# Kernel tuning notes

Hardware: AMD Instinct MI355X
Metric: run time of the kernel (lower is better)

## Reference

```python
import jax, jax.numpy as jnp
import numpy as np

CHANNELS = 256
TEMPERATURE = 0.1
VAR_LAMBDA = 0.001
N = 4096


def _pairwise_sq_dist(x, y):
    xx = jnp.sum(x * x, axis=-1)[:, None]
    yy = jnp.sum(y * y, axis=-1)[None, :]
    xy = jnp.einsum('ic,jc->ij', x, y)
    return xx + yy - 2.0 * xy


def _tcc_loss(emb_a, emb_b, idxes):
    scale = 1.0 / (CHANNELS * TEMPERATURE)
    sim_ab = -_pairwise_sq_dist(emb_a, emb_b) * scale            # [Na, Nb]
    softmaxed_sim_ab = jax.nn.softmax(sim_ab, axis=-1)
    soft_nn = softmaxed_sim_ab @ emb_b                            # [Na, C]
    sim_ba = -_pairwise_sq_dist(soft_nn, emb_a) * scale           # [Na, Na]
    beta = jax.nn.softmax(sim_ba, axis=-1)
    preds = jnp.sum(beta * idxes, axis=-1, keepdims=True)         # [Na, 1]
    pred_var = jnp.sum((idxes - preds) ** 2 * beta, axis=1)       # [Na]
    pred_var_log = jnp.log(pred_var)
    squared_error = (idxes - jnp.squeeze(preds, -1)) ** 2
    return jnp.sum(jnp.exp(-pred_var_log) * squared_error + VAR_LAMBDA * pred_var_log)


def setup_inputs() -> dict:
    key = jax.random.key(0)
    k1, k2 = jax.random.split(key)
    emb_a = jax.random.normal(k1, (1, N, CHANNELS), dtype=jnp.float32)
    emb_b = jax.random.normal(k2, (1, N, CHANNELS), dtype=jnp.float32)
    idx_a = jnp.arange(N, dtype=jnp.float32)
    idx_b = jnp.arange(N, dtype=jnp.float32)
    return {"emb_a": emb_a, "emb_b": emb_b, "idx_a": idx_a, "idx_b": idx_b}


def reference(emb_a, emb_b, idx_a, idx_b):
    a = jnp.squeeze(emb_a, 0)
    b = jnp.squeeze(emb_b, 0)
    loss_ab = _tcc_loss(a, b, idx_a)
    loss_ba = _tcc_loss(b, a, idx_b)
    return (loss_ab + loss_ba) / (a.shape[0] + b.shape[0])
```

## Files before the change

kernel.cpp:

```cpp
#include <hip/hip_runtime.h>

#define NTOT 4096
#define CH 256
#define SCALE 0.0390625f
#define LAM 0.001f

typedef unsigned short u16;
typedef __attribute__((ext_vector_type(8))) short short8;
typedef __attribute__((ext_vector_type(4))) float floatx4;

__device__ __forceinline__ float wave_sum64(float v) {
  #pragma unroll
  for (int o = 32; o; o >>= 1) v += __shfl_down(v, o, 64);
  return v;
}
__device__ __forceinline__ u16 f2bf(float f) {
  unsigned u = __float_as_uint(f);
  u += 0x7fffu + ((u >> 16) & 1u);
  return (u16)(u >> 16);
}
__device__ __forceinline__ float bf2f(u16 h) {
  return __uint_as_float(((unsigned)h) << 16);
}
__device__ __forceinline__ void gload_lds(const u16* g, void* l) {
  __builtin_amdgcn_global_load_lds((const __attribute__((address_space(1))) void*)g,
                                   (__attribute__((address_space(3))) void*)l, 16, 0, 0);
}
__device__ __forceinline__ void mm4x4(const short8 (&av)[4], const short8 (&bv)[4],
                                      floatx4 (&acc)[4][4]) {
  #pragma unroll
  for (int m = 0; m < 4; ++m)
    #pragma unroll
    for (int n = 0; n < 4; ++n)
      acc[m][n] = __builtin_amdgcn_mfma_f32_16x16x32_bf16(av[m], bv[n], acc[m][n], 0, 0, 0);
}

__global__ __launch_bounds__(64) void cvt_norm_k(const float* __restrict__ a,
                                                 const float* __restrict__ b,
                                                 u16* __restrict__ ab, u16* __restrict__ bb,
                                                 float* __restrict__ na, float* __restrict__ nb) {
  int row = blockIdx.x;
  const float* src; u16* dst; float* nd;
  if (row < NTOT) { src = a; dst = ab; nd = na; }
  else { row -= NTOT; src = b; dst = bb; nd = nb; }
  const float4 v = *reinterpret_cast<const float4*>(src + (size_t)row * CH + threadIdx.x * 4);
  const u16 h0 = f2bf(v.x), h1 = f2bf(v.y), h2 = f2bf(v.z), h3 = f2bf(v.w);
  uint2 st;
  st.x = (unsigned)h0 | ((unsigned)h1 << 16);
  st.y = (unsigned)h2 | ((unsigned)h3 << 16);
  *reinterpret_cast<uint2*>(dst + (size_t)row * CH + threadIdx.x * 4) = st;
  const float f0 = bf2f(h0), f1 = bf2f(h1), f2 = bf2f(h2), f3 = bf2f(h3);
  float s = f0 * f0 + f1 * f1 + f2 * f2 + f3 * f3;
  s = wave_sum64(s);
  if (threadIdx.x == 0) nd[row] = s;
}

__global__ __launch_bounds__(256) void transpose2_k(const u16* __restrict__ ab,
                                                    const u16* __restrict__ bb,
                                                    u16* __restrict__ at, u16* __restrict__ bt) {
  const u16* __restrict__ src = blockIdx.z ? bb : ab;
  u16* __restrict__ dst = blockIdx.z ? bt : at;
  __shared__ u16 t[32][33];
  const int bx = blockIdx.x * 32, by = blockIdx.y * 32;
  const int lx = threadIdx.x & 31, ly = threadIdx.x >> 5;
  #pragma unroll
  for (int i = 0; i < 32; i += 8)
    t[ly + i][lx] = src[(size_t)(by + ly + i) * CH + bx + lx];
  __syncthreads();
  #pragma unroll
  for (int i = 0; i < 32; i += 8)
    dst[(size_t)(bx + ly + i) * NTOT + by + lx] = t[lx][ly + i];
}

__global__ __launch_bounds__(256, 2) void gemm_exp_k(const u16* __restrict__ abf,
                                                     const u16* __restrict__ bbf,
                                                     const float* __restrict__ na,
                                                     const float* __restrict__ nb,
                                                     u16* __restrict__ E,
                                                     float* __restrict__ dnp) {
  const int dir = blockIdx.z;
  const u16* __restrict__ A = dir ? bbf : abf;
  const u16* __restrict__ B = dir ? abf : bbf;
  const float* __restrict__ ny = dir ? na : nb;
  E += (size_t)dir * NTOT * NTOT;
  dnp += (size_t)dir * NTOT * 64;

  __shared__ u16 As[2][128][64];
  __shared__ u16 Bs[2][128][64];
  const int tid = threadIdx.x, wid = tid >> 6, lane = tid & 63;
  const int bn = blockIdx.x * 128, bm = blockIdx.y * 128;
  const int wr = (wid >> 1) * 64, wc = (wid & 1) * 64;
  const int lr = lane & 15;

  auto stage = [&](int t, int bi) {
    const int k0 = t * 64;
    #pragma unroll
    for (int i = 0; i < 4; ++i) {
      const int lb = (wid + 4 * i) * 1024;
      const int db = lb + lane * 16;
      const int r = db >> 7;
      const int cb = (db & 127) ^ ((r & 7) << 4);
      gload_lds(A + (size_t)(bm + r) * CH + k0 + (cb >> 1), (char*)&As[bi][0][0] + lb);
      gload_lds(B + (size_t)(bn + r) * CH + k0 + (cb >> 1), (char*)&Bs[bi][0][0] + lb);
    }
  };

  floatx4 acc[4][4] = {};
  stage(0, 0);
  asm volatile("s_waitcnt vmcnt(0)" ::: "memory");
  __builtin_amdgcn_s_barrier();
  #pragma unroll
  for (int t = 0; t < 4; ++t) {
    if (t < 3) stage(t + 1, (t + 1) & 1);
    const int bi = t & 1;
    const char* Ab = (const char*)&As[bi][0][0];
    const char* Bb = (const char*)&Bs[bi][0][0];
    #pragma unroll
    for (int ks = 0; ks < 2; ++ks) {
      const int ob = ks * 64 + (lane >> 4) * 16;
      short8 af[4], bfr[4];
      #pragma unroll
      for (int m = 0; m < 4; ++m) {
        const int row = wr + m * 16 + lr;
        af[m] = *reinterpret_cast<const short8*>(Ab + row * 128 + (ob ^ ((row & 7) << 4)));
      }
      #pragma unroll
      for (int n = 0; n < 4; ++n) {
        const int row = wc + n * 16 + lr;
        bfr[n] = *reinterpret_cast<const short8*>(Bb + row * 128 + (ob ^ ((row & 7) << 4)));
      }
      mm4x4(af, bfr, acc);
    }
    if (t < 3) {
      asm volatile("s_waitcnt vmcnt(0)" ::: "memory");
      __builtin_amdgcn_s_barrier();
    }
  }
  float nyv[4];
  #pragma unroll
  for (int n = 0; n < 4; ++n) nyv[n] = ny[bn + wc + n * 16 + lr];
  float rowsum[4][4] = {};
  #pragma unroll
  for (int m = 0; m < 4; ++m) {
    const int rowb = bm + wr + m * 16 + (lane >> 4) * 4;
    #pragma unroll
    for (int n = 0; n < 4; ++n) {
      const int col = bn + wc + n * 16 + lr;
      #pragma unroll
      for (int r = 0; r < 4; ++r) {
        const float w = __expf((2.f * acc[m][n][r] - nyv[n]) * SCALE);
        E[(size_t)(rowb + r) * NTOT + col] = f2bf(w);
        rowsum[m][r] += w;
      }
    }
  }
  #pragma unroll
  for (int m = 0; m < 4; ++m) {
    const int rowb = bm + wr + m * 16 + (lane >> 4) * 4;
    #pragma unroll
    for (int r = 0; r < 4; ++r) {
      float s = rowsum[m][r];
      #pragma unroll
      for (int o = 1; o < 16; o <<= 1) s += __shfl_xor(s, o, 64);
      if (lr == 0) dnp[(size_t)(rowb + r) * 64 + blockIdx.x * 2 + (wid & 1)] = s;
    }
  }
}

__global__ __launch_bounds__(256, 2) void gemm_qp_k(const u16* __restrict__ E,
                                                    const u16* __restrict__ att,
                                                    const u16* __restrict__ btt,
                                                    float* __restrict__ Qp) {
  const int dir = blockIdx.z >> 2, kz = blockIdx.z & 3;
  const u16* __restrict__ A = E + (size_t)dir * NTOT * NTOT;
  const u16* __restrict__ B = dir ? att : btt;
  float* __restrict__ C = Qp + (size_t)dir * 4 * NTOT * CH + (size_t)kz * NTOT * CH;
  const int k0base = kz * (NTOT / 4);

  __shared__ u16 As[2][128][64];
  __shared__ u16 Bs[2][128][64];
  const int tid = threadIdx.x, wid = tid >> 6, lane = tid & 63;
  const int bn = blockIdx.x * 128, bm = blockIdx.y * 128;
  const int wr = (wid >> 1) * 64, wc = (wid & 1) * 64;
  const int lr = lane & 15;

  auto stage = [&](int t, int bi) {
    const int k0 = k0base + t * 64;
    #pragma unroll
    for (int i = 0; i < 4; ++i) {
      const int lb = (wid + 4 * i) * 1024;
      const int db = lb + lane * 16;
      const int r = db >> 7;
      const int cb = (db & 127) ^ ((r & 7) << 4);
      gload_lds(A + (size_t)(bm + r) * NTOT + k0 + (cb >> 1), (char*)&As[bi][0][0] + lb);
      gload_lds(B + (size_t)(bn + r) * NTOT + k0 + (cb >> 1), (char*)&Bs[bi][0][0] + lb);
    }
  };

  floatx4 acc[4][4] = {};
  stage(0, 0);
  asm volatile("s_waitcnt vmcnt(0)" ::: "memory");
  __builtin_amdgcn_s_barrier();
  for (int t = 0; t < 16; ++t) {
    if (t < 15) stage(t + 1, (t + 1) & 1);
    const int bi = t & 1;
    const char* Ab = (const char*)&As[bi][0][0];
    const char* Bb = (const char*)&Bs[bi][0][0];
    #pragma unroll
    for (int ks = 0; ks < 2; ++ks) {
      const int ob = ks * 64 + (lane >> 4) * 16;
      short8 af[4], bfr[4];
      #pragma unroll
      for (int m = 0; m < 4; ++m) {
        const int row = wr + m * 16 + lr;
        af[m] = *reinterpret_cast<const short8*>(Ab + row * 128 + (ob ^ ((row & 7) << 4)));
      }
      #pragma unroll
      for (int n = 0; n < 4; ++n) {
        const int row = wc + n * 16 + lr;
        bfr[n] = *reinterpret_cast<const short8*>(Bb + row * 128 + (ob ^ ((row & 7) << 4)));
      }
      mm4x4(af, bfr, acc);
    }
    asm volatile("s_waitcnt vmcnt(0)" ::: "memory");
    __builtin_amdgcn_s_barrier();
  }
  #pragma unroll
  for (int m = 0; m < 4; ++m) {
    const int row = bm + wr + m * 16 + (lane >> 4) * 4;
    #pragma unroll
    for (int n = 0; n < 4; ++n) {
      const int col = bn + wc + n * 16 + lr;
      #pragma unroll
      for (int r = 0; r < 4; ++r)
        C[(size_t)(row + r) * CH + col] = acc[m][n][r];
    }
  }
}

__global__ __launch_bounds__(256) void reduce_q_k(const float* __restrict__ Qp,
                                                  const float* __restrict__ dnp,
                                                  u16* __restrict__ Qb) {
  const int dir = blockIdx.z;
  Qp += (size_t)dir * 4 * NTOT * CH;
  dnp += (size_t)dir * NTOT * 64;
  Qb += (size_t)dir * NTOT * CH;
  const int row = blockIdx.x, tid = threadIdx.x;
  __shared__ float sdn;
  if (tid < 64) {
    float s = dnp[(size_t)row * 64 + tid];
    s = wave_sum64(s);
    if (tid == 0) sdn = 1.0f / s;
  }
  __syncthreads();
  const float rdn = sdn;
  const size_t o = (size_t)row * CH + tid;
  const size_t st = (size_t)NTOT * CH;
  const float q = (Qp[o] + Qp[o + st] + Qp[o + 2 * st] + Qp[o + 3 * st]) * rdn;
  Qb[o] = f2bf(q);
}

__global__ __launch_bounds__(256, 2) void flash_stats_k(const u16* __restrict__ Qball,
                                                        const u16* __restrict__ abf,
                                                        const u16* __restrict__ bbf,
                                                        const float* __restrict__ na,
                                                        const float* __restrict__ nb,
                                                        const float* __restrict__ idxa,
                                                        const float* __restrict__ idxb,
                                                        float4* __restrict__ statsp) {
  const int dir = blockIdx.z;
  const u16* __restrict__ Qb = Qball + (size_t)dir * NTOT * CH;
  const u16* __restrict__ X = dir ? bbf : abf;
  const float* __restrict__ nx = dir ? nb : na;
  const float* __restrict__ idx = dir ? idxb : idxa;
  statsp += (size_t)dir * NTOT * 32;

  __shared__ u16 As[2][128][64];
  __shared__ u16 Bs[2][128][64];
  const int tid = threadIdx.x, wid = tid >> 6, lane = tid & 63;
  const int bm = blockIdx.y * 128;
  const int jbase = blockIdx.x * 256;
  const int wr = (wid >> 1) * 64, wc = (wid & 1) * 64;
  const int lr = lane & 15;

  auto stage = [&](int t, int bi) {
    const int k0 = (t & 3) * 64;
    const int bn = jbase + (t >> 2) * 128;
    #pragma unroll
    for (int i = 0; i < 4; ++i) {
      const int lb = (wid + 4 * i) * 1024;
      const int db = lb + lane * 16;
      const int r = db >> 7;
      const int cb = (db & 127) ^ ((r & 7) << 4);
      gload_lds(Qb + (size_t)(bm + r) * CH + k0 + (cb >> 1), (char*)&As[bi][0][0] + lb);
      gload_lds(X + (size_t)(bn + r) * CH + k0 + (cb >> 1), (char*)&Bs[bi][0][0] + lb);
    }
  };

  float cen[4][4];
  #pragma unroll
  for (int m = 0; m < 4; ++m) {
    const int rowb = bm + wr + m * 16 + (lane >> 4) * 4;
    #pragma unroll
    for (int r = 0; r < 4; ++r) cen[m][r] = idx[rowb + r];
  }
  float s0[4][4] = {}, s1[4][4] = {}, s2[4][4] = {};
  floatx4 acc[4][4] = {};

  stage(0, 0);
  asm volatile("s_waitcnt vmcnt(0)" ::: "memory");
  __builtin_amdgcn_s_barrier();
  #pragma unroll
  for (int t = 0; t < 8; ++t) {
    if (t < 7) stage(t + 1, (t + 1) & 1);
    const int bi = t & 1;
    const char* Ab = (const char*)&As[bi][0][0];
    const char* Bb = (const char*)&Bs[bi][0][0];
    #pragma unroll
    for (int ks = 0; ks < 2; ++ks) {
      const int ob = ks * 64 + (lane >> 4) * 16;
      short8 af[4], bfr[4];
      #pragma unroll
      for (int m = 0; m < 4; ++m) {
        const int row = wr + m * 16 + lr;
        af[m] = *reinterpret_cast<const short8*>(Ab + row * 128 + (ob ^ ((row & 7) << 4)));
      }
      #pragma unroll
      for (int n = 0; n < 4; ++n) {
        const int row = wc + n * 16 + lr;
        bfr[n] = *reinterpret_cast<const short8*>(Bb + row * 128 + (ob ^ ((row & 7) << 4)));
      }
      mm4x4(af, bfr, acc);
    }
    if ((t & 3) == 3) {
      const int bn = jbase + (t >> 2) * 128;
      #pragma unroll
      for (int n = 0; n < 4; ++n) {
        const int col = bn + wc + n * 16 + lr;
        const float nxv = nx[col];
        const float iv = idx[col];
        #pragma unroll
        for (int m = 0; m < 4; ++m) {
          #pragma unroll
          for (int r = 0; r < 4; ++r) {
            const float w = __expf((2.f * acc[m][n][r] - nxv) * SCALE);
            const float d = iv - cen[m][r];
            s0[m][r] += w;
            s1[m][r] += w * d;
            s2[m][r] += w * d * d;
            acc[m][n][r] = 0.f;
          }
        }
      }
    }
    if (t < 7) {
      asm volatile("s_waitcnt vmcnt(0)" ::: "memory");
      __builtin_amdgcn_s_barrier();
    }
  }
  #pragma unroll
  for (int m = 0; m < 4; ++m) {
    const int rowb = bm + wr + m * 16 + (lane >> 4) * 4;
    #pragma unroll
    for (int r = 0; r < 4; ++r) {
      float a = s0[m][r], b = s1[m][r], c = s2[m][r];
      #pragma unroll
      for (int o = 1; o < 16; o <<= 1) {
        a += __shfl_xor(a, o, 64);
        b += __shfl_xor(b, o, 64);
        c += __shfl_xor(c, o, 64);
      }
      if (lr == 0)
        statsp[(size_t)(rowb + r) * 32 + blockIdx.x * 2 + (wid & 1)] = make_float4(a, b, c, 0.f);
    }
  }
}

__global__ __launch_bounds__(256) void stats_combine_k(const float4* __restrict__ statsp,
                                                       float* __restrict__ terms) {
  const int row = blockIdx.x * 256 + threadIdx.x;
  float S0 = 0.f, S1 = 0.f, S2 = 0.f;
  #pragma unroll
  for (int p = 0; p < 32; ++p) {
    const float4 v = statsp[(size_t)row * 32 + p];
    S0 += v.x; S1 += v.y; S2 += v.z;
  }
  const float mu = S1 / S0;
  const float var = S2 / S0 - mu * mu;
  terms[row] = mu * mu / var + LAM * logf(var);
}

__global__ __launch_bounds__(256) void final_reduce_k(const float* __restrict__ terms,
                                                      float* __restrict__ out) {
  float s = 0.f;
  for (int i = threadIdx.x; i < 2 * NTOT; i += 256) s += terms[i];
  __shared__ float red[4];
  s = wave_sum64(s);
  if ((threadIdx.x & 63) == 0) red[threadIdx.x >> 6] = s;
  __syncthreads();
  if (threadIdx.x == 0) out[0] = (red[0] + red[1] + red[2] + red[3]) * (1.0f / (2.0f * NTOT));
}

extern "C" void kernel_launch(void* const* d_in, const int* in_sizes, int n_in,
                              void* d_out, int out_size, void* d_ws, size_t ws_size,
                              hipStream_t stream) {
  const float* a    = (const float*)d_in[0];
  const float* b    = (const float*)d_in[1];
  const float* idxa = (const float*)d_in[2];
  const float* idxb = (const float*)d_in[3];
  float* out = (float*)d_out;
  char* ws = (char*)d_ws;

  size_t off = 0;
  u16*    E    = (u16*)(ws + off);    off += 2 * (size_t)NTOT * NTOT * 2;
  float*  Qp   = (float*)(ws + off);  off += 2 * 4 * (size_t)NTOT * CH * 4;
  u16*    Qb   = (u16*)(ws + off);    off += 2 * (size_t)NTOT * CH * 2;
  u16*    abf  = (u16*)(ws + off);    off += (size_t)NTOT * CH * 2;
  u16*    bbf  = (u16*)(ws + off);    off += (size_t)NTOT * CH * 2;
  u16*    att  = (u16*)(ws + off);    off += (size_t)NTOT * CH * 2;
  u16*    btt  = (u16*)(ws + off);    off += (size_t)NTOT * CH * 2;
  float*  na   = (float*)(ws + off);  off += (size_t)NTOT * 4;
  float*  nb   = (float*)(ws + off);  off += (size_t)NTOT * 4;
  float*  dnp  = (float*)(ws + off);  off += 2 * (size_t)NTOT * 64 * 4;
  float4* stp  = (float4*)(ws + off); off += 2 * (size_t)NTOT * 32 * 16;
  float*  terms = (float*)(ws + off);

  cvt_norm_k<<<2 * NTOT, 64, 0, stream>>>(a, b, abf, bbf, na, nb);
  transpose2_k<<<dim3(CH / 32, NTOT / 32, 2), 256, 0, stream>>>(abf, bbf, att, btt);
  gemm_exp_k<<<dim3(NTOT / 128, NTOT / 128, 2), 256, 0, stream>>>(abf, bbf, na, nb, E, dnp);
  gemm_qp_k<<<dim3(CH / 128, NTOT / 128, 8), 256, 0, stream>>>(E, att, btt, Qp);
  reduce_q_k<<<dim3(NTOT, 1, 2), 256, 0, stream>>>(Qp, dnp, Qb);
  flash_stats_k<<<dim3(16, NTOT / 128, 2), 256, 0, stream>>>(Qb, abf, bbf, na, nb,
                                                             idxa, idxb, stp);
  stats_combine_k<<<2 * NTOT / 256, 256, 0, stream>>>(stp, terms);
  final_reduce_k<<<1, 256, 0, stream>>>(terms, out);
}
```

Before: 137.1 us.

## Drop LDS double-buffering for higher occupancy and split QP GEMM K eight ways

```diff
diff --git a/kernel.cpp b/kernel.cpp
--- a/kernel.cpp
+++ b/kernel.cpp
@@ -72,7 +72,7 @@
     dst[(size_t)(bx + ly + i) * NTOT + by + lx] = t[lx][ly + i];
 }
 
-__global__ __launch_bounds__(256, 2) void gemm_exp_k(const u16* __restrict__ abf,
+__global__ __launch_bounds__(256, 4) void gemm_exp_k(const u16* __restrict__ abf,
                                                      const u16* __restrict__ bbf,
                                                      const float* __restrict__ na,
                                                      const float* __restrict__ nb,
@@ -85,14 +85,17 @@
   E += (size_t)dir * NTOT * NTOT;
   dnp += (size_t)dir * NTOT * 64;
 
-  __shared__ u16 As[2][128][64];
-  __shared__ u16 Bs[2][128][64];
+  __shared__ u16 As[128][64];
+  __shared__ u16 Bs[128][64];
   const int tid = threadIdx.x, wid = tid >> 6, lane = tid & 63;
   const int bn = blockIdx.x * 128, bm = blockIdx.y * 128;
   const int wr = (wid >> 1) * 64, wc = (wid & 1) * 64;
   const int lr = lane & 15;
 
-  auto stage = [&](int t, int bi) {
+  floatx4 acc[4][4] = {};
+  #pragma unroll
+  for (int t = 0; t < 4; ++t) {
+    if (t) __syncthreads();
     const int k0 = t * 64;
     #pragma unroll
     for (int i = 0; i < 4; ++i) {
@@ -100,21 +103,12 @@
       const int db = lb + lane * 16;
       const int r = db >> 7;
       const int cb = (db & 127) ^ ((r & 7) << 4);
-      gload_lds(A + (size_t)(bm + r) * CH + k0 + (cb >> 1), (char*)&As[bi][0][0] + lb);
-      gload_lds(B + (size_t)(bn + r) * CH + k0 + (cb >> 1), (char*)&Bs[bi][0][0] + lb);
-    }
-  };
-
-  floatx4 acc[4][4] = {};
-  stage(0, 0);
-  asm volatile("s_waitcnt vmcnt(0)" ::: "memory");
-  __builtin_amdgcn_s_barrier();
-  #pragma unroll
-  for (int t = 0; t < 4; ++t) {
-    if (t < 3) stage(t + 1, (t + 1) & 1);
-    const int bi = t & 1;
-    const char* Ab = (const char*)&As[bi][0][0];
-    const char* Bb = (const char*)&Bs[bi][0][0];
+      gload_lds(A + (size_t)(bm + r) * CH + k0 + (cb >> 1), (char*)&As[0][0] + lb);
+      gload_lds(B + (size_t)(bn + r) * CH + k0 + (cb >> 1), (char*)&Bs[0][0] + lb);
+    }
+    __syncthreads();
+    const char* Ab = (const char*)&As[0][0];
+    const char* Bb = (const char*)&Bs[0][0];
     #pragma unroll
     for (int ks = 0; ks < 2; ++ks) {
       const int ob = ks * 64 + (lane >> 4) * 16;
@@ -130,10 +124,6 @@
         bfr[n] = *reinterpret_cast<const short8*>(Bb + row * 128 + (ob ^ ((row & 7) << 4)));
       }
       mm4x4(af, bfr, acc);
-    }
-    if (t < 3) {
-      asm volatile("s_waitcnt vmcnt(0)" ::: "memory");
-      __builtin_amdgcn_s_barrier();
     }
   }
   float nyv[4];
@@ -167,24 +157,26 @@
   }
 }
 
-__global__ __launch_bounds__(256, 2) void gemm_qp_k(const u16* __restrict__ E,
+__global__ __launch_bounds__(256, 4) void gemm_qp_k(const u16* __restrict__ E,
                                                     const u16* __restrict__ att,
                                                     const u16* __restrict__ btt,
                                                     float* __restrict__ Qp) {
-  const int dir = blockIdx.z >> 2, kz = blockIdx.z & 3;
+  const int dir = blockIdx.z >> 3, kz = blockIdx.z & 7;
   const u16* __restrict__ A = E + (size_t)dir * NTOT * NTOT;
   const u16* __restrict__ B = dir ? att : btt;
-  float* __restrict__ C = Qp + (size_t)dir * 4 * NTOT * CH + (size_t)kz * NTOT * CH;
-  const int k0base = kz * (NTOT / 4);
-
-  __shared__ u16 As[2][128][64];
-  __shared__ u16 Bs[2][128][64];
+  float* __restrict__ C = Qp + (size_t)dir * 8 * NTOT * CH + (size_t)kz * NTOT * CH;
+  const int k0base = kz * (NTOT / 8);
+
+  __shared__ u16 As[128][64];
+  __shared__ u16 Bs[128][64];
   const int tid = threadIdx.x, wid = tid >> 6, lane = tid & 63;
   const int bn = blockIdx.x * 128, bm = blockIdx.y * 128;
   const int wr = (wid >> 1) * 64, wc = (wid & 1) * 64;
   const int lr = lane & 15;
 
-  auto stage = [&](int t, int bi) {
+  floatx4 acc[4][4] = {};
+  for (int t = 0; t < 8; ++t) {
+    if (t) __syncthreads();
     const int k0 = k0base + t * 64;
     #pragma unroll
     for (int i = 0; i < 4; ++i) {
@@ -192,20 +184,12 @@
       const int db = lb + lane * 16;
       const int r = db >> 7;
       const int cb = (db & 127) ^ ((r & 7) << 4);
-      gload_lds(A + (size_t)(bm + r) * NTOT + k0 + (cb >> 1), (char*)&As[bi][0][0] + lb);
-      gload_lds(B + (size_t)(bn + r) * NTOT + k0 + (cb >> 1), (char*)&Bs[bi][0][0] + lb);
-    }
-  };
-
-  floatx4 acc[4][4] = {};
-  stage(0, 0);
-  asm volatile("s_waitcnt vmcnt(0)" ::: "memory");
-  __builtin_amdgcn_s_barrier();
-  for (int t = 0; t < 16; ++t) {
-    if (t < 15) stage(t + 1, (t + 1) & 1);
-    const int bi = t & 1;
-    const char* Ab = (const char*)&As[bi][0][0];
-    const char* Bb = (const char*)&Bs[bi][0][0];
+      gload_lds(A + (size_t)(bm + r) * NTOT + k0 + (cb >> 1), (char*)&As[0][0] + lb);
+      gload_lds(B + (size_t)(bn + r) * NTOT + k0 + (cb >> 1), (char*)&Bs[0][0] + lb);
+    }
+    __syncthreads();
+    const char* Ab = (const char*)&As[0][0];
+    const char* Bb = (const char*)&Bs[0][0];
     #pragma unroll
     for (int ks = 0; ks < 2; ++ks) {
       const int ob = ks * 64 + (lane >> 4) * 16;
@@ -222,8 +206,6 @@
       }
       mm4x4(af, bfr, acc);
     }
-    asm volatile("s_waitcnt vmcnt(0)" ::: "memory");
-    __builtin_amdgcn_s_barrier();
   }
   #pragma unroll
   for (int m = 0; m < 4; ++m) {
@@ -242,7 +224,7 @@
                                                   const float* __restrict__ dnp,
                                                   u16* __restrict__ Qb) {
   const int dir = blockIdx.z;
-  Qp += (size_t)dir * 4 * NTOT * CH;
+  Qp += (size_t)dir * 8 * NTOT * CH;
   dnp += (size_t)dir * NTOT * 64;
   Qb += (size_t)dir * NTOT * CH;
   const int row = blockIdx.x, tid = threadIdx.x;
@@ -256,11 +238,13 @@
   const float rdn = sdn;
   const size_t o = (size_t)row * CH + tid;
   const size_t st = (size_t)NTOT * CH;
-  const float q = (Qp[o] + Qp[o + st] + Qp[o + 2 * st] + Qp[o + 3 * st]) * rdn;
-  Qb[o] = f2bf(q);
-}
-
-__global__ __launch_bounds__(256, 2) void flash_stats_k(const u16* __restrict__ Qball,
+  float q = 0.f;
+  #pragma unroll
+  for (int p = 0; p < 8; ++p) q += Qp[o + p * st];
+  Qb[o] = f2bf(q * rdn);
+}
+
+__global__ __launch_bounds__(256, 4) void flash_stats_k(const u16* __restrict__ Qball,
                                                         const u16* __restrict__ abf,
                                                         const u16* __restrict__ bbf,
                                                         const float* __restrict__ na,
@@ -275,15 +259,27 @@
   const float* __restrict__ idx = dir ? idxb : idxa;
   statsp += (size_t)dir * NTOT * 32;
 
-  __shared__ u16 As[2][128][64];
-  __shared__ u16 Bs[2][128][64];
+  __shared__ u16 As[128][64];
+  __shared__ u16 Bs[128][64];
   const int tid = threadIdx.x, wid = tid >> 6, lane = tid & 63;
   const int bm = blockIdx.y * 128;
   const int jbase = blockIdx.x * 256;
   const int wr = (wid >> 1) * 64, wc = (wid & 1) * 64;
   const int lr = lane & 15;
 
-  auto stage = [&](int t, int bi) {
+  float cen[4][4];
+  #pragma unroll
+  for (int m = 0; m < 4; ++m) {
+    const int rowb = bm + wr + m * 16 + (lane >> 4) * 4;
+    #pragma unroll
+    for (int r = 0; r < 4; ++r) cen[m][r] = idx[rowb + r];
+  }
+  float s0[4][4] = {}, s1[4][4] = {}, s2[4][4] = {};
+  floatx4 acc[4][4] = {};
+
+  #pragma unroll
+  for (int t = 0; t < 8; ++t) {
+    if (t) __syncthreads();
     const int k0 = (t & 3) * 64;
     const int bn = jbase + (t >> 2) * 128;
     #pragma unroll
@@ -292,30 +288,12 @@
       const int db = lb + lane * 16;
       const int r = db >> 7;
       const int cb = (db & 127) ^ ((r & 7) << 4);
-      gload_lds(Qb + (size_t)(bm + r) * CH + k0 + (cb >> 1), (char*)&As[bi][0][0] + lb);
-      gload_lds(X + (size_t)(bn + r) * CH + k0 + (cb >> 1), (char*)&Bs[bi][0][0] + lb);
-    }
-  };
-
-  float cen[4][4];
-  #pragma unroll
-  for (int m = 0; m < 4; ++m) {
-    const int rowb = bm + wr + m * 16 + (lane >> 4) * 4;
-    #pragma unroll
-    for (int r = 0; r < 4; ++r) cen[m][r] = idx[rowb + r];
-  }
-  float s0[4][4] = {}, s1[4][4] = {}, s2[4][4] = {};
-  floatx4 acc[4][4] = {};
-
-  stage(0, 0);
-  asm volatile("s_waitcnt vmcnt(0)" ::: "memory");
-  __builtin_amdgcn_s_barrier();
-  #pragma unroll
-  for (int t = 0; t < 8; ++t) {
-    if (t < 7) stage(t + 1, (t + 1) & 1);
-    const int bi = t & 1;
-    const char* Ab = (const char*)&As[bi][0][0];
-    const char* Bb = (const char*)&Bs[bi][0][0];
+      gload_lds(Qb + (size_t)(bm + r) * CH + k0 + (cb >> 1), (char*)&As[0][0] + lb);
+      gload_lds(X + (size_t)(bn + r) * CH + k0 + (cb >> 1), (char*)&Bs[0][0] + lb);
+    }
+    __syncthreads();
+    const char* Ab = (const char*)&As[0][0];
+    const char* Bb = (const char*)&Bs[0][0];
     #pragma unroll
     for (int ks = 0; ks < 2; ++ks) {
       const int ob = ks * 64 + (lane >> 4) * 16;
@@ -333,10 +311,10 @@
       mm4x4(af, bfr, acc);
     }
     if ((t & 3) == 3) {
-      const int bn = jbase + (t >> 2) * 128;
+      const int bn2 = jbase + (t >> 2) * 128;
       #pragma unroll
       for (int n = 0; n < 4; ++n) {
-        const int col = bn + wc + n * 16 + lr;
+        const int col = bn2 + wc + n * 16 + lr;
         const float nxv = nx[col];
         const float iv = idx[col];
         #pragma unroll
@@ -353,10 +331,6 @@
         }
       }
     }
-    if (t < 7) {
-      asm volatile("s_waitcnt vmcnt(0)" ::: "memory");
-      __builtin_amdgcn_s_barrier();
-    }
   }
   #pragma unroll
   for (int m = 0; m < 4; ++m) {
@@ -413,7 +387,7 @@
 
   size_t off = 0;
   u16*    E    = (u16*)(ws + off);    off += 2 * (size_t)NTOT * NTOT * 2;
-  float*  Qp   = (float*)(ws + off);  off += 2 * 4 * (size_t)NTOT * CH * 4;
+  float*  Qp   = (float*)(ws + off);  off += 2 * 8 * (size_t)NTOT * CH * 4;
   u16*    Qb   = (u16*)(ws + off);    off += 2 * (size_t)NTOT * CH * 2;
   u16*    abf  = (u16*)(ws + off);    off += (size_t)NTOT * CH * 2;
   u16*    bbf  = (u16*)(ws + off);    off += (size_t)NTOT * CH * 2;
@@ -428,7 +402,7 @@
   cvt_norm_k<<<2 * NTOT, 64, 0, stream>>>(a, b, abf, bbf, na, nb);
   transpose2_k<<<dim3(CH / 32, NTOT / 32, 2), 256, 0, stream>>>(abf, bbf, att, btt);
   gemm_exp_k<<<dim3(NTOT / 128, NTOT / 128, 2), 256, 0, stream>>>(abf, bbf, na, nb, E, dnp);
-  gemm_qp_k<<<dim3(CH / 128, NTOT / 128, 8), 256, 0, stream>>>(E, att, btt, Qp);
+  gemm_qp_k<<<dim3(CH / 128, NTOT / 128, 16), 256, 0, stream>>>(E, att, btt, Qp);
   reduce_q_k<<<dim3(NTOT, 1, 2), 256, 0, stream>>>(Qp, dnp, Qb);
   flash_stats_k<<<dim3(16, NTOT / 128, 2), 256, 0, stream>>>(Qb, abf, bbf, na, nb,
                                                              idxa, idxb, stp);
```

After: 189.1 us. +37.9%, slower.

## Halve K-tile LDS footprint and split flash_stats over more blocks for occupancy

Applied to the files above, without the earlier changes.

```diff
diff --git a/kernel.cpp b/kernel.cpp
--- a/kernel.cpp
+++ b/kernel.cpp
@@ -34,6 +34,7 @@
     for (int n = 0; n < 4; ++n)
       acc[m][n] = __builtin_amdgcn_mfma_f32_16x16x32_bf16(av[m], bv[n], acc[m][n], 0, 0, 0);
 }
+__device__ __forceinline__ int swz64(int row) { return ((row >> 1) & 3) << 4; }
 
 __global__ __launch_bounds__(64) void cvt_norm_k(const float* __restrict__ a,
                                                  const float* __restrict__ b,
@@ -72,7 +73,7 @@
     dst[(size_t)(bx + ly + i) * NTOT + by + lx] = t[lx][ly + i];
 }
 
-__global__ __launch_bounds__(256, 2) void gemm_exp_k(const u16* __restrict__ abf,
+__global__ __launch_bounds__(256, 4) void gemm_exp_k(const u16* __restrict__ abf,
                                                      const u16* __restrict__ bbf,
                                                      const float* __restrict__ na,
                                                      const float* __restrict__ nb,
@@ -85,21 +86,21 @@
   E += (size_t)dir * NTOT * NTOT;
   dnp += (size_t)dir * NTOT * 64;
 
-  __shared__ u16 As[2][128][64];
-  __shared__ u16 Bs[2][128][64];
+  __shared__ u16 As[2][128][32];
+  __shared__ u16 Bs[2][128][32];
   const int tid = threadIdx.x, wid = tid >> 6, lane = tid & 63;
   const int bn = blockIdx.x * 128, bm = blockIdx.y * 128;
   const int wr = (wid >> 1) * 64, wc = (wid & 1) * 64;
-  const int lr = lane & 15;
+  const int lr = lane & 15, g = lane >> 4;
 
   auto stage = [&](int t, int bi) {
-    const int k0 = t * 64;
-    #pragma unroll
-    for (int i = 0; i < 4; ++i) {
+    const int k0 = t * 32;
+    #pragma unroll
+    for (int i = 0; i < 2; ++i) {
       const int lb = (wid + 4 * i) * 1024;
       const int db = lb + lane * 16;
-      const int r = db >> 7;
-      const int cb = (db & 127) ^ ((r & 7) << 4);
+      const int r = db >> 6;
+      const int cb = (db & 63) ^ swz64(r);
       gload_lds(A + (size_t)(bm + r) * CH + k0 + (cb >> 1), (char*)&As[bi][0][0] + lb);
       gload_lds(B + (size_t)(bn + r) * CH + k0 + (cb >> 1), (char*)&Bs[bi][0][0] + lb);
     }
@@ -110,28 +111,24 @@
   asm volatile("s_waitcnt vmcnt(0)" ::: "memory");
   __builtin_amdgcn_s_barrier();
   #pragma unroll
-  for (int t = 0; t < 4; ++t) {
-    if (t < 3) stage(t + 1, (t + 1) & 1);
+  for (int t = 0; t < 8; ++t) {
+    if (t < 7) stage(t + 1, (t + 1) & 1);
     const int bi = t & 1;
     const char* Ab = (const char*)&As[bi][0][0];
     const char* Bb = (const char*)&Bs[bi][0][0];
-    #pragma unroll
-    for (int ks = 0; ks < 2; ++ks) {
-      const int ob = ks * 64 + (lane >> 4) * 16;
-      short8 af[4], bfr[4];
-      #pragma unroll
-      for (int m = 0; m < 4; ++m) {
-        const int row = wr + m * 16 + lr;
-        af[m] = *reinterpret_cast<const short8*>(Ab + row * 128 + (ob ^ ((row & 7) << 4)));
-      }
-      #pragma unroll
-      for (int n = 0; n < 4; ++n) {
-        const int row = wc + n * 16 + lr;
-        bfr[n] = *reinterpret_cast<const short8*>(Bb + row * 128 + (ob ^ ((row & 7) << 4)));
-      }
-      mm4x4(af, bfr, acc);
-    }
-    if (t < 3) {
+    short8 af[4], bfr[4];
+    #pragma unroll
+    for (int m = 0; m < 4; ++m) {
+      const int row = wr + m * 16 + lr;
+      af[m] = *reinterpret_cast<const short8*>(Ab + row * 64 + ((g * 16) ^ swz64(row)));
+    }
+    #pragma unroll
+    for (int n = 0; n < 4; ++n) {
+      const int row = wc + n * 16 + lr;
+      bfr[n] = *reinterpret_cast<const short8*>(Bb + row * 64 + ((g * 16) ^ swz64(row)));
+    }
+    mm4x4(af, bfr, acc);
+    if (t < 7) {
       asm volatile("s_waitcnt vmcnt(0)" ::: "memory");
       __builtin_amdgcn_s_barrier();
     }
@@ -142,7 +139,7 @@
   float rowsum[4][4] = {};
   #pragma unroll
   for (int m = 0; m < 4; ++m) {
-    const int rowb = bm + wr + m * 16 + (lane >> 4) * 4;
+    const int rowb = bm + wr + m * 16 + g * 4;
     #pragma unroll
     for (int n = 0; n < 4; ++n) {
       const int col = bn + wc + n * 16 + lr;
@@ -156,7 +153,7 @@
   }
   #pragma unroll
   for (int m = 0; m < 4; ++m) {
-    const int rowb = bm + wr + m * 16 + (lane >> 4) * 4;
+    const int rowb = bm + wr + m * 16 + g * 4;
     #pragma unroll
     for (int r = 0; r < 4; ++r) {
       float s = rowsum[m][r];
@@ -167,7 +164,7 @@
   }
 }
 
-__global__ __launch_bounds__(256, 2) void gemm_qp_k(const u16* __restrict__ E,
+__global__ __launch_bounds__(256, 4) void gemm_qp_k(const u16* __restrict__ E,
                                                     const u16* __restrict__ att,
                                                     const u16* __restrict__ btt,
                                                     float* __restrict__ Qp) {
@@ -177,21 +174,21 @@
   float* __restrict__ C = Qp + (size_t)dir * 4 * NTOT * CH + (size_t)kz * NTOT * CH;
   const int k0base = kz * (NTOT / 4);
 
-  __shared__ u16 As[2][128][64];
-  __shared__ u16 Bs[2][128][64];
+  __shared__ u16 As[2][128][32];
+  __shared__ u16 Bs[2][128][32];
   const int tid = threadIdx.x, wid = tid >> 6, lane = tid & 63;
   const int bn = blockIdx.x * 128, bm = blockIdx.y * 128;
   const int wr = (wid >> 1) * 64, wc = (wid & 1) * 64;
-  const int lr = lane & 15;
+  const int lr = lane & 15, g = lane >> 4;
 
   auto stage = [&](int t, int bi) {
-    const int k0 = k0base + t * 64;
-    #pragma unroll
-    for (int i = 0; i < 4; ++i) {
+    const int k0 = k0base + t * 32;
+    #pragma unroll
+    for (int i = 0; i < 2; ++i) {
       const int lb = (wid + 4 * i) * 1024;
       const int db = lb + lane * 16;
-      const int r = db >> 7;
-      const int cb = (db & 127) ^ ((r & 7) << 4);
+      const int r = db >> 6;
+      const int cb = (db & 63) ^ swz64(r);
       gload_lds(A + (size_t)(bm + r) * NTOT + k0 + (cb >> 1), (char*)&As[bi][0][0] + lb);
       gload_lds(B + (size_t)(bn + r) * NTOT + k0 + (cb >> 1), (char*)&Bs[bi][0][0] + lb);
     }
@@ -201,33 +198,29 @@
   stage(0, 0);
   asm volatile("s_waitcnt vmcnt(0)" ::: "memory");
   __builtin_amdgcn_s_barrier();
-  for (int t = 0; t < 16; ++t) {
-    if (t < 15) stage(t + 1, (t + 1) & 1);
+  for (int t = 0; t < 32; ++t) {
+    if (t < 31) stage(t + 1, (t + 1) & 1);
     const int bi = t & 1;
     const char* Ab = (const char*)&As[bi][0][0];
     const char* Bb = (const char*)&Bs[bi][0][0];
-    #pragma unroll
-    for (int ks = 0; ks < 2; ++ks) {
-      const int ob = ks * 64 + (lane >> 4) * 16;
-      short8 af[4], bfr[4];
-      #pragma unroll
-      for (int m = 0; m < 4; ++m) {
-        const int row = wr + m * 16 + lr;
-        af[m] = *reinterpret_cast<const short8*>(Ab + row * 128 + (ob ^ ((row & 7) << 4)));
-      }
-      #pragma unroll
-      for (int n = 0; n < 4; ++n) {
-        const int row = wc + n * 16 + lr;
-        bfr[n] = *reinterpret_cast<const short8*>(Bb + row * 128 + (ob ^ ((row & 7) << 4)));
-      }
-      mm4x4(af, bfr, acc);
-    }
+    short8 af[4], bfr[4];
+    #pragma unroll
+    for (int m = 0; m < 4; ++m) {
+      const int row = wr + m * 16 + lr;
+      af[m] = *reinterpret_cast<const short8*>(Ab + row * 64 + ((g * 16) ^ swz64(row)));
+    }
+    #pragma unroll
+    for (int n = 0; n < 4; ++n) {
+      const int row = wc + n * 16 + lr;
+      bfr[n] = *reinterpret_cast<const short8*>(Bb + row * 64 + ((g * 16) ^ swz64(row)));
+    }
+    mm4x4(af, bfr, acc);
     asm volatile("s_waitcnt vmcnt(0)" ::: "memory");
     __builtin_amdgcn_s_barrier();
   }
   #pragma unroll
   for (int m = 0; m < 4; ++m) {
-    const int row = bm + wr + m * 16 + (lane >> 4) * 4;
+    const int row = bm + wr + m * 16 + g * 4;
     #pragma unroll
     for (int n = 0; n < 4; ++n) {
       const int col = bn + wc + n * 16 + lr;
@@ -260,7 +253,7 @@
   Qb[o] = f2bf(q);
 }
 
-__global__ __launch_bounds__(256, 2) void flash_stats_k(const u16* __restrict__ Qball,
+__global__ __launch_bounds__(256, 4) void flash_stats_k(const u16* __restrict__ Qball,
                                                         const u16* __restrict__ abf,
                                                         const u16* __restrict__ bbf,
                                                         const float* __restrict__ na,
@@ -273,40 +266,30 @@
   const u16* __restrict__ X = dir ? bbf : abf;
   const float* __restrict__ nx = dir ? nb : na;
   const float* __restrict__ idx = dir ? idxb : idxa;
-  statsp += (size_t)dir * NTOT * 32;
-
-  __shared__ u16 As[2][128][64];
-  __shared__ u16 Bs[2][128][64];
+  statsp += (size_t)dir * NTOT * 64;
+
+  __shared__ u16 As[2][128][32];
+  __shared__ u16 Bs[2][128][32];
   const int tid = threadIdx.x, wid = tid >> 6, lane = tid & 63;
   const int bm = blockIdx.y * 128;
-  const int jbase = blockIdx.x * 256;
+  const int bn = blockIdx.x * 128;
   const int wr = (wid >> 1) * 64, wc = (wid & 1) * 64;
-  const int lr = lane & 15;
+  const int lr = lane & 15, g = lane >> 4;
 
   auto stage = [&](int t, int bi) {
-    const int k0 = (t & 3) * 64;
-    const int bn = jbase + (t >> 2) * 128;
-    #pragma unroll
-    for (int i = 0; i < 4; ++i) {
+    const int k0 = t * 32;
+    #pragma unroll
+    for (int i = 0; i < 2; ++i) {
       const int lb = (wid + 4 * i) * 1024;
       const int db = lb + lane * 16;
-      const int r = db >> 7;
-      const int cb = (db & 127) ^ ((r & 7) << 4);
+      const int r = db >> 6;
+      const int cb = (db & 63) ^ swz64(r);
       gload_lds(Qb + (size_t)(bm + r) * CH + k0 + (cb >> 1), (char*)&As[bi][0][0] + lb);
       gload_lds(X + (size_t)(bn + r) * CH + k0 + (cb >> 1), (char*)&Bs[bi][0][0] + lb);
     }
   };
 
-  float cen[4][4];
-  #pragma unroll
-  for (int m = 0; m < 4; ++m) {
-    const int rowb = bm + wr + m * 16 + (lane >> 4) * 4;
-    #pragma unroll
-    for (int r = 0; r < 4; ++r) cen[m][r] = idx[rowb + r];
-  }
-  float s0[4][4] = {}, s1[4][4] = {}, s2[4][4] = {};
   floatx4 acc[4][4] = {};
-
   stage(0, 0);
   asm volatile("s_waitcnt vmcnt(0)" ::: "memory");
   __builtin_amdgcn_s_barrier();
@@ -316,51 +299,51 @@
     const int bi = t & 1;
     const char* Ab = (const char*)&As[bi][0][0];
     const char* Bb = (const char*)&Bs[bi][0][0];
-    #pragma unroll
-    for (int ks = 0; ks < 2; ++ks) {
-      const int ob = ks * 64 + (lane >> 4) * 16;
-      short8 af[4], bfr[4];
-      #pragma unroll
-      for (int m = 0; m < 4; ++m) {
-        const int row = wr + m * 16 + lr;
-        af[m] = *reinterpret_cast<const short8*>(Ab + row * 128 + (ob ^ ((row & 7) << 4)));
-      }
-      #pragma unroll
-      for (int n = 0; n < 4; ++n) {
-        const int row = wc + n * 16 + lr;
-        bfr[n] = *reinterpret_cast<const short8*>(Bb + row * 128 + (ob ^ ((row & 7) << 4)));
-      }
-      mm4x4(af, bfr, acc);
-    }
-    if ((t & 3) == 3) {
-      const int bn = jbase + (t >> 2) * 128;
-      #pragma unroll
-      for (int n = 0; n < 4; ++n) {
-        const int col = bn + wc + n * 16 + lr;
-        const float nxv = nx[col];
-        const float iv = idx[col];
-        #pragma unroll
-        for (int m = 0; m < 4; ++m) {
-          #pragma unroll
-          for (int r = 0; r < 4; ++r) {
-            const float w = __expf((2.f * acc[m][n][r] - nxv) * SCALE);
-            const float d = iv - cen[m][r];
-            s0[m][r] += w;
-            s1[m][r] += w * d;
-            s2[m][r] += w * d * d;
-            acc[m][n][r] = 0.f;
-          }
-        }
-      }
-    }
+    short8 af[4], bfr[4];
+    #pragma unroll
+    for (int m = 0; m < 4; ++m) {
+      const int row = wr + m * 16 + lr;
+      af[m] = *reinterpret_cast<const short8*>(Ab + row * 64 + ((g * 16) ^ swz64(row)));
+    }
+    #pragma unroll
+    for (int n = 0; n < 4; ++n) {
+      const int row = wc + n * 16 + lr;
+      bfr[n] = *reinterpret_cast<const short8*>(Bb + row * 64 + ((g * 16) ^ swz64(row)));
+    }
+    mm4x4(af, bfr, acc);
     if (t < 7) {
       asm volatile("s_waitcnt vmcnt(0)" ::: "memory");
       __builtin_amdgcn_s_barrier();
     }
   }
+  float cen[4][4];
   #pragma unroll
   for (int m = 0; m < 4; ++m) {
-    const int rowb = bm + wr + m * 16 + (lane >> 4) * 4;
+    const int rowb = bm + wr + m * 16 + g * 4;
+    #pragma unroll
+    for (int r = 0; r < 4; ++r) cen[m][r] = idx[rowb + r];
+  }
+  float s0[4][4] = {}, s1[4][4] = {}, s2[4][4] = {};
+  #pragma unroll
+  for (int n = 0; n < 4; ++n) {
+    const int col = bn + wc + n * 16 + lr;
+    const float nxv = nx[col];
+    const float iv = idx[col];
+    #pragma unroll
+    for (int m = 0; m < 4; ++m) {
+      #pragma unroll
+      for (int r = 0; r < 4; ++r) {
+        const float w = __expf((2.f * acc[m][n][r] - nxv) * SCALE);
+        const float d = iv - cen[m][r];
+        s0[m][r] += w;
+        s1[m][r] += w * d;
+        s2[m][r] += w * d * d;
+      }
+    }
+  }
+  #pragma unroll
+  for (int m = 0; m < 4; ++m) {
+    const int rowb = bm + wr + m * 16 + g * 4;
     #pragma unroll
     for (int r = 0; r < 4; ++r) {
       float a = s0[m][r], b = s1[m][r], c = s2[m][r];
@@ -371,7 +354,7 @@
         c += __shfl_xor(c, o, 64);
       }
       if (lr == 0)
-        statsp[(size_t)(rowb + r) * 32 + blockIdx.x * 2 + (wid & 1)] = make_float4(a, b, c, 0.f);
+        statsp[(size_t)(rowb + r) * 64 + blockIdx.x * 2 + (wid & 1)] = make_float4(a, b, c, 0.f);
     }
   }
 }
@@ -381,8 +364,8 @@
   const int row = blockIdx.x * 256 + threadIdx.x;
   float S0 = 0.f, S1 = 0.f, S2 = 0.f;
   #pragma unroll
-  for (int p = 0; p < 32; ++p) {
-    const float4 v = statsp[(size_t)row * 32 + p];
+  for (int p = 0; p < 64; ++p) {
+    const float4 v = statsp[(size_t)row * 64 + p];
     S0 += v.x; S1 += v.y; S2 += v.z;
   }
   const float mu = S1 / S0;
@@ -422,7 +405,7 @@
   float*  na   = (float*)(ws + off);  off += (size_t)NTOT * 4;
   float*  nb   = (float*)(ws + off);  off += (size_t)NTOT * 4;
   float*  dnp  = (float*)(ws + off);  off += 2 * (size_t)NTOT * 64 * 4;
-  float4* stp  = (float4*)(ws + off); off += 2 * (size_t)NTOT * 32 * 16;
+  float4* stp  = (float4*)(ws + off); off += 2 * (size_t)NTOT * 64 * 16;
   float*  terms = (float*)(ws + off);
 
   cvt_norm_k<<<2 * NTOT, 64, 0, stream>>>(a, b, abf, bbf, na, nb);
@@ -430,8 +413,8 @@
   gemm_exp_k<<<dim3(NTOT / 128, NTOT / 128, 2), 256, 0, stream>>>(abf, bbf, na, nb, E, dnp);
   gemm_qp_k<<<dim3(CH / 128, NTOT / 128, 8), 256, 0, stream>>>(E, att, btt, Qp);
   reduce_q_k<<<dim3(NTOT, 1, 2), 256, 0, stream>>>(Qp, dnp, Qb);
-  flash_stats_k<<<dim3(16, NTOT / 128, 2), 256, 0, stream>>>(Qb, abf, bbf, na, nb,
-                                                             idxa, idxb, stp);
+  flash_stats_k<<<dim3(NTOT / 128, NTOT / 128, 2), 256, 0, stream>>>(Qb, abf, bbf, na, nb,
+                                                                     idxa, idxb, stp);
   stats_combine_k<<<2 * NTOT / 256, 256, 0, stream>>>(stp, terms);
   final_reduce_k<<<1, 256, 0, stream>>>(terms, out);
 }
```

Result: slower. 152.9 us (+11.5%).

## Remap workgroup IDs to tiles for XCD-aware L2 locality in GEMM kernels

Applied to the files above, without the earlier changes.

```diff
diff --git a/kernel.cpp b/kernel.cpp
--- a/kernel.cpp
+++ b/kernel.cpp
@@ -78,7 +78,14 @@
                                                      const float* __restrict__ nb,
                                                      u16* __restrict__ E,
                                                      float* __restrict__ dnp) {
-  const int dir = blockIdx.z;
+  const int wg = blockIdx.x;
+  const int dir = wg >> 10;
+  const int w = wg & 1023;
+  const int xcd = w & 7;
+  const int local = w >> 3;
+  const int bx = local & 31;
+  const int by = xcd * 4 + (local >> 5);
+
   const u16* __restrict__ A = dir ? bbf : abf;
   const u16* __restrict__ B = dir ? abf : bbf;
   const float* __restrict__ ny = dir ? na : nb;
@@ -88,7 +95,7 @@
   __shared__ u16 As[2][128][64];
   __shared__ u16 Bs[2][128][64];
   const int tid = threadIdx.x, wid = tid >> 6, lane = tid & 63;
-  const int bn = blockIdx.x * 128, bm = blockIdx.y * 128;
+  const int bn = bx * 128, bm = by * 128;
   const int wr = (wid >> 1) * 64, wc = (wid & 1) * 64;
   const int lr = lane & 15;
 
@@ -162,7 +169,7 @@
       float s = rowsum[m][r];
       #pragma unroll
       for (int o = 1; o < 16; o <<= 1) s += __shfl_xor(s, o, 64);
-      if (lr == 0) dnp[(size_t)(rowb + r) * 64 + blockIdx.x * 2 + (wid & 1)] = s;
+      if (lr == 0) dnp[(size_t)(rowb + r) * 64 + bx * 2 + (wid & 1)] = s;
     }
   }
 }
@@ -171,7 +178,12 @@
                                                     const u16* __restrict__ att,
                                                     const u16* __restrict__ btt,
                                                     float* __restrict__ Qp) {
-  const int dir = blockIdx.z >> 2, kz = blockIdx.z & 3;
+  const int wg = blockIdx.x;
+  const int dk = wg & 7;
+  const int j = wg >> 3;
+  const int dir = dk >> 2, kz = dk & 3;
+  const int bxi = j & 1, byi = j >> 1;
+
   const u16* __restrict__ A = E + (size_t)dir * NTOT * NTOT;
   const u16* __restrict__ B = dir ? att : btt;
   float* __restrict__ C = Qp + (size_t)dir * 4 * NTOT * CH + (size_t)kz * NTOT * CH;
@@ -180,7 +192,7 @@
   __shared__ u16 As[2][128][64];
   __shared__ u16 Bs[2][128][64];
   const int tid = threadIdx.x, wid = tid >> 6, lane = tid & 63;
-  const int bn = blockIdx.x * 128, bm = blockIdx.y * 128;
+  const int bn = bxi * 128, bm = byi * 128;
   const int wr = (wid >> 1) * 64, wc = (wid & 1) * 64;
   const int lr = lane & 15;
 
@@ -268,7 +280,14 @@
                                                         const float* __restrict__ idxa,
                                                         const float* __restrict__ idxb,
                                                         float4* __restrict__ statsp) {
-  const int dir = blockIdx.z;
+  const int wg = blockIdx.x;
+  const int dir = wg >> 9;
+  const int w = wg & 511;
+  const int xcd = w & 7;
+  const int local = w >> 3;
+  const int bx = local & 15;
+  const int by = xcd * 4 + (local >> 4);
+
   const u16* __restrict__ Qb = Qball + (size_t)dir * NTOT * CH;
   const u16* __restrict__ X = dir ? bbf : abf;
   const float* __restrict__ nx = dir ? nb : na;
@@ -278,8 +297,8 @@
   __shared__ u16 As[2][128][64];
   __shared__ u16 Bs[2][128][64];
   const int tid = threadIdx.x, wid = tid >> 6, lane = tid & 63;
-  const int bm = blockIdx.y * 128;
-  const int jbase = blockIdx.x * 256;
+  const int bm = by * 128;
+  const int jbase = bx * 256;
   const int wr = (wid >> 1) * 64, wc = (wid & 1) * 64;
   const int lr = lane & 15;
 
@@ -371,7 +390,7 @@
         c += __shfl_xor(c, o, 64);
       }
       if (lr == 0)
-        statsp[(size_t)(rowb + r) * 32 + blockIdx.x * 2 + (wid & 1)] = make_float4(a, b, c, 0.f);
+        statsp[(size_t)(rowb + r) * 32 + bx * 2 + (wid & 1)] = make_float4(a, b, c, 0.f);
     }
   }
 }
@@ -427,11 +446,10 @@
 
   cvt_norm_k<<<2 * NTOT, 64, 0, stream>>>(a, b, abf, bbf, na, nb);
   transpose2_k<<<dim3(CH / 32, NTOT / 32, 2), 256, 0, stream>>>(abf, bbf, att, btt);
-  gemm_exp_k<<<dim3(NTOT / 128, NTOT / 128, 2), 256, 0, stream>>>(abf, bbf, na, nb, E, dnp);
-  gemm_qp_k<<<dim3(CH / 128, NTOT / 128, 8), 256, 0, stream>>>(E, att, btt, Qp);
+  gemm_exp_k<<<2048, 256, 0, stream>>>(abf, bbf, na, nb, E, dnp);
+  gemm_qp_k<<<512, 256, 0, stream>>>(E, att, btt, Qp);
   reduce_q_k<<<dim3(NTOT, 1, 2), 256, 0, stream>>>(Qp, dnp, Qb);
-  flash_stats_k<<<dim3(16, NTOT / 128, 2), 256, 0, stream>>>(Qb, abf, bbf, na, nb,
-                                                             idxa, idxb, stp);
+  flash_stats_k<<<1024, 256, 0, stream>>>(Qb, abf, bbf, na, nb, idxa, idxb, stp);
   stats_combine_k<<<2 * NTOT / 256, 256, 0, stream>>>(stp, terms);
   final_reduce_k<<<1, 256, 0, stream>>>(terms, out);
 }
```

Result: no change. 135.9 us (-0.9%).
